# Kernel optimization log

Hardware: AMD Instinct MI355X
Metric: run time of the kernel (lower is better)

The kernel has to match this reference:

```python
import jax, jax.numpy as jnp
import numpy as np

IN_DIMS = [16, 16, 16]
OUT_DIMS = [16, 16, 16]
RANKS = [1, 16, 16, 1]
BATCH = 1024


def setup_inputs() -> dict:
    key = jax.random.key(0)
    ks = jax.random.split(key, 1 + len(IN_DIMS))
    vector = jax.random.normal(ks[0], (BATCH, *IN_DIMS), dtype=jnp.float32)
    inp = {"vector": vector}
    for i in range(len(IN_DIMS)):
        shape = (RANKS[i], OUT_DIMS[i], IN_DIMS[i], RANKS[i + 1])
        scale = 1.0 / float(np.sqrt(RANKS[i] * IN_DIMS[i]))
        inp[f"core{i}"] = jax.random.normal(ks[1 + i], shape, dtype=jnp.float32) * scale
    return inp


def _tt_matvec(vector, cores):
    """y = M @ x where M is the TT/MPO matrix defined by `cores`.

    vector: (B, d_in_1, ..., d_in_d). Returns (B, d_out_1, ..., d_out_d).
    Mirrors TTMatrix.metric_projection exactly (output dims absorbed into batch).
    """
    bs0 = vector.shape[0]
    res = vector[:, None]  # (B, r0=1, d_in_1, ..., d_in_d)
    bs = bs0
    for core in cores:
        r, o, i, k = core.shape
        rem = res.shape[3:]  # remaining un-contracted input dims
        res_t = res.reshape(bs, r, i, -1)  # (bs, r, i, x)
        # contract rank-in and input dim: (r,o,i,k),(b,r,i,x) -> (b,k,o,x)
        new = jnp.einsum('roik,brix->bkox', core, res_t)
        new = jnp.transpose(new, (0, 2, 1, 3)).reshape(bs * o, k, *rem)
        bs = bs * o
        res = new
    res = jnp.squeeze(res, axis=-1)  # last rank is 1
    out_dims = [c.shape[1] for c in cores]
    return res.reshape(bs0, *out_dims)


def reference(vector, core0, core1, core2):
    return _tt_matvec(vector, (core0, core1, core2))
```

## Files before the change

kernel.cpp:

```cpp
#include <hip/hip_runtime.h>
#include <hip/hip_bf16.h>


typedef short bf16x8 __attribute__((ext_vector_type(8)));
typedef float f32x4 __attribute__((ext_vector_type(4)));

#define WS_A1_OFF 0
#define WS_A0_OFF 131072
#define WS_A2_OFF 147456
#define WS_NEEDED 155648

__device__ __forceinline__ unsigned short f2bf(float f) {
    union { float f; unsigned int u; } x; x.f = f;
    unsigned int u = x.u;
    u += 0x7fffu + ((u >> 16) & 1u);
    return (unsigned short)(u >> 16);
}

__device__ __forceinline__ unsigned int pk_bf16(float lo, float hi) {
    __hip_bfloat162 h = __float22bfloat162_rn(make_float2(lo, hi));
    unsigned int r;
    __builtin_memcpy(&r, &h, 4);
    return r;
}

__global__ void tt_repack(const float* __restrict__ c0,
                          const float* __restrict__ c1,
                          const float* __restrict__ c2,
                          unsigned short* __restrict__ ws) {
    int idx = blockIdx.x * 256 + threadIdx.x;
    if (idx < 8192) {
        int o2 = idx >> 9, ks = (idx >> 6) & 7, l = idx & 63;
        int k2 = l & 15;
        unsigned short* dst = ws + ((size_t)(o2 * 8 + ks) * 64 + l) * 8;
        #pragma unroll
        for (int j = 0; j < 8; ++j) {
            int k = ks * 32 + ((l >> 4) * 8) + j;
            dst[j] = f2bf(c1[(k & 15) * 4096 + o2 * 256 + (k >> 4) * 16 + k2]);
        }
    } else if (idx < 9216) {
        int t = idx - 8192;
        int o1 = t >> 6, l = t & 63;
        unsigned short* dst = ws + WS_A0_OFF / 2 + ((size_t)o1 * 64 + l) * 8;
        #pragma unroll
        for (int j = 0; j < 8; ++j) {
            int k = ((l >> 4) * 8) + j;
            float v = (l < 32) ? c0[o1 * 256 + k * 16 + (l & 15)] : 0.f;
            dst[j] = f2bf(v);
        }
    } else if (idx < 9728) {
        int t = idx - 9216;
        int ks = t >> 6, l = t & 63;
        unsigned short* dst = ws + WS_A2_OFF / 2 + ((size_t)ks * 64 + l) * 8;
        #pragma unroll
        for (int j = 0; j < 8; ++j) {
            int k = ks * 32 + ((l >> 4) * 8) + j;
            dst[j] = f2bf(c2[(k & 15) * 256 + (l & 15) * 16 + (k >> 4)]);
        }
    }
}

template <bool PACKED>
__global__ __launch_bounds__(512, 4) void tt_main(
    const float* __restrict__ vg, const float* __restrict__ c0,
    const float* __restrict__ c1, const float* __restrict__ c2,
    const unsigned short* __restrict__ ws, float* __restrict__ outg)
{
    __shared__ unsigned short T1[16384];
    __shared__ unsigned short T2[16384];

    const int b   = blockIdx.x;
    const int t   = threadIdx.x;
    const int w   = t >> 6;
    const int l   = t & 63;
    const int l15 = l & 15;
    const int lg  = l >> 4;

    bf16x8 fb0[2];
    {
        const float* vb = vg + (size_t)b * 4096;
        #pragma unroll
        for (int nt = 0; nt < 2; ++nt) {
            bf16x8 f = {0, 0, 0, 0, 0, 0, 0, 0};
            if (l < 32) {
                int i2 = 2 * w + nt;
                const float* p = vb + (lg * 8) * 256 + i2 * 16 + l15;
                #pragma unroll
                for (int j = 0; j < 8; ++j) f[j] = (short)f2bf(p[j * 256]);
            }
            fb0[nt] = f;
        }
    }
    bf16x8 fa2[8];
    if constexpr (PACKED) {
        #pragma unroll
        for (int ks = 0; ks < 8; ++ks)
            fa2[ks] = *(const bf16x8*)(ws + WS_A2_OFF / 2 + ((size_t)ks * 64 + l) * 8);
    } else {
        for (int ks = 0; ks < 8; ++ks) {
            bf16x8 f;
            for (int j = 0; j < 8; ++j) {
                int k = ks * 32 + lg * 8 + j;
                f[j] = (short)f2bf(c2[(k & 15) * 256 + l15 * 16 + (k >> 4)]);
            }
            fa2[ks] = f;
        }
    }

    const unsigned short* a1p = PACKED ? (ws + (size_t)l * 8) : nullptr;

    for (int nc = 0; nc < 4; ++nc) {
        #pragma unroll
        for (int mtl = 0; mtl < 4; ++mtl) {
            const int o1 = nc * 4 + mtl;
            bf16x8 fa0;
            if constexpr (PACKED) {
                fa0 = *(const bf16x8*)(ws + WS_A0_OFF / 2 + ((size_t)o1 * 64 + l) * 8);
            } else {
                bf16x8 f = {0, 0, 0, 0, 0, 0, 0, 0};
                if (l < 32) {
                    #pragma unroll
                    for (int j = 0; j < 8; ++j)
                        f[j] = (short)f2bf(c0[o1 * 256 + (lg * 8 + j) * 16 + l15]);
                }
                fa0 = f;
            }
            #pragma unroll
            for (int nt = 0; nt < 2; ++nt) {
                f32x4 z = {0.f, 0.f, 0.f, 0.f};
                f32x4 d = __builtin_amdgcn_mfma_f32_16x16x32_bf16(fa0, fb0[nt], z, 0, 0, 0);
                const int i2 = 2 * w + nt;
                const int n  = mtl * 16 + l15;
                int byte = (n * 512 + (i2 * 16 + lg * 4) * 2) ^ ((l15 & 7) << 4);
                uint2 wv;
                wv.x = pk_bf16(d[0], d[1]);
                wv.y = pk_bf16(d[2], d[3]);
                *(uint2*)((char*)T1 + byte) = wv;
            }
        }
        __syncthreads();

        {
            f32x4 acc[2][4];
            #pragma unroll
            for (int rt = 0; rt < 2; ++rt)
                #pragma unroll
                for (int nt = 0; nt < 4; ++nt) acc[rt][nt] = (f32x4){0.f, 0.f, 0.f, 0.f};

            #pragma unroll 2
            for (int ks = 0; ks < 8; ++ks) {
                bf16x8 fa_0, fa_1;
                if constexpr (PACKED) {
                    fa_0 = *(const bf16x8*)(a1p + ((2 * w + 0) * 8 + ks) * 512);
                    fa_1 = *(const bf16x8*)(a1p + ((2 * w + 1) * 8 + ks) * 512);
                } else {
                    bf16x8 ftmp[2];
                    for (int rt = 0; rt < 2; ++rt) {
                        int o2 = 2 * w + rt;
                        bf16x8 f;
                        for (int j = 0; j < 8; ++j) {
                            int k = ks * 32 + lg * 8 + j;
                            f[j] = (short)f2bf(c1[(k & 15) * 4096 + o2 * 256 + (k >> 4) * 16 + l15]);
                        }
                        ftmp[rt] = f;
                    }
                    fa_0 = ftmp[0]; fa_1 = ftmp[1];
                }
                #pragma unroll
                for (int nt = 0; nt < 4; ++nt) {
                    int byte = ((nt * 16 + l15) * 512 + (ks * 32 + lg * 8) * 2) ^ ((l15 & 7) << 4);
                    bf16x8 fb = *(const bf16x8*)((char*)T1 + byte);
                    acc[0][nt] = __builtin_amdgcn_mfma_f32_16x16x32_bf16(fa_0, fb, acc[0][nt], 0, 0, 0);
                    acc[1][nt] = __builtin_amdgcn_mfma_f32_16x16x32_bf16(fa_1, fb, acc[1][nt], 0, 0, 0);
                }
            }
            #pragma unroll
            for (int rt = 0; rt < 2; ++rt) {
                const int o2 = 2 * w + rt;
                #pragma unroll
                for (int nt = 0; nt < 4; ++nt) {
                    int byte = ((nt * 16 + o2) * 512 + (l15 * 16 + lg * 4) * 2) ^ ((o2 & 7) << 4);
                    uint2 wv;
                    wv.x = pk_bf16(acc[rt][nt][0], acc[rt][nt][1]);
                    wv.y = pk_bf16(acc[rt][nt][2], acc[rt][nt][3]);
                    *(uint2*)((char*)T2 + byte) = wv;
                }
            }
        }
        __syncthreads();

        if (w < 4) {
            f32x4 acc3 = {0.f, 0.f, 0.f, 0.f};
            #pragma unroll
            for (int ks = 0; ks < 8; ++ks) {
                int byte = ((w * 16 + l15) * 512 + (ks * 32 + lg * 8) * 2) ^ ((l15 & 7) << 4);
                bf16x8 fb = *(const bf16x8*)((char*)T2 + byte);
                acc3 = __builtin_amdgcn_mfma_f32_16x16x32_bf16(fa2[ks], fb, acc3, 0, 0, 0);
            }
            float* ob = outg + (size_t)b * 4096;
            *(f32x4*)(ob + (nc * 4 + w) * 256 + l15 * 16 + lg * 4) = acc3;
        }
        __syncthreads();
    }
}

extern "C" void kernel_launch(void* const* d_in, const int* in_sizes, int n_in,
                              void* d_out, int out_size, void* d_ws, size_t ws_size,
                              hipStream_t stream) {
    const float* vg  = (const float*)d_in[0];
    const float* c0g = (const float*)d_in[1];
    const float* c1g = (const float*)d_in[2];
    const float* c2g = (const float*)d_in[3];
    float* outg = (float*)d_out;

    const int B = in_sizes[0] / 4096;
    const bool packed = (ws_size >= (size_t)WS_NEEDED) && (d_ws != nullptr);

    if (packed) {
        tt_repack<<<dim3(38), dim3(256), 0, stream>>>(c0g, c1g, c2g, (unsigned short*)d_ws);
        tt_main<true><<<dim3(B), dim3(512), 0, stream>>>(
            vg, c0g, c1g, c2g, (const unsigned short*)d_ws, outg);
    } else {
        tt_main<false><<<dim3(B), dim3(512), 0, stream>>>(
            vg, c0g, c1g, c2g, nullptr, outg);
    }
}
```

Measured before the change: 53.98 us.

## Double-buffer T2, preload core1/core0 fragments, drop trailing barrier

Makes T2 double-buffered so the third stage of one chunk can overlap with the first stage of the next, which lets the trailing __syncthreads be removed. All core1 and core0 fragments for a chunk are now loaded into registers up front, before the MFMA loops, and the stage-2 loop is fully unrolled. Stage 3 splits its accumulation into two independent chains to shorten the MFMA dependency chain. In exchange, register use rises (occupancy hint lowered from 4 to 2 blocks) and LDS use rises by 32KB, which reduces resident blocks per CU.

```diff
diff --git a/kernel.cpp b/kernel.cpp
--- a/kernel.cpp
+++ b/kernel.cpp
@@ -61,13 +61,13 @@
 }
 
 template <bool PACKED>
-__global__ __launch_bounds__(512, 4) void tt_main(
+__global__ __launch_bounds__(512, 2) void tt_main(
     const float* __restrict__ vg, const float* __restrict__ c0,
     const float* __restrict__ c1, const float* __restrict__ c2,
     const unsigned short* __restrict__ ws, float* __restrict__ outg)
 {
     __shared__ unsigned short T1[16384];
-    __shared__ unsigned short T2[16384];
+    __shared__ unsigned short T2[2][16384];
 
     const int b   = blockIdx.x;
     const int t   = threadIdx.x;
@@ -110,25 +110,47 @@
     const unsigned short* a1p = PACKED ? (ws + (size_t)l * 8) : nullptr;
 
     for (int nc = 0; nc < 4; ++nc) {
-        #pragma unroll
-        for (int mtl = 0; mtl < 4; ++mtl) {
-            const int o1 = nc * 4 + mtl;
-            bf16x8 fa0;
-            if constexpr (PACKED) {
-                fa0 = *(const bf16x8*)(ws + WS_A0_OFF / 2 + ((size_t)o1 * 64 + l) * 8);
-            } else {
+        unsigned short* T2c = T2[nc & 1];
+
+        bf16x8 fa1p[16];
+        bf16x8 fa0p[4];
+        if constexpr (PACKED) {
+            #pragma unroll
+            for (int ks = 0; ks < 8; ++ks) {
+                fa1p[ks]     = *(const bf16x8*)(a1p + ((2 * w + 0) * 8 + ks) * 512);
+                fa1p[8 + ks] = *(const bf16x8*)(a1p + ((2 * w + 1) * 8 + ks) * 512);
+            }
+            #pragma unroll
+            for (int mtl = 0; mtl < 4; ++mtl)
+                fa0p[mtl] = *(const bf16x8*)(ws + WS_A0_OFF / 2 +
+                                             ((size_t)(nc * 4 + mtl) * 64 + l) * 8);
+        } else {
+            for (int rt = 0; rt < 2; ++rt)
+                for (int ks = 0; ks < 8; ++ks) {
+                    int o2 = 2 * w + rt;
+                    bf16x8 f;
+                    for (int j = 0; j < 8; ++j) {
+                        int k = ks * 32 + lg * 8 + j;
+                        f[j] = (short)f2bf(c1[(k & 15) * 4096 + o2 * 256 + (k >> 4) * 16 + l15]);
+                    }
+                    fa1p[rt * 8 + ks] = f;
+                }
+            for (int mtl = 0; mtl < 4; ++mtl) {
                 bf16x8 f = {0, 0, 0, 0, 0, 0, 0, 0};
                 if (l < 32) {
-                    #pragma unroll
                     for (int j = 0; j < 8; ++j)
-                        f[j] = (short)f2bf(c0[o1 * 256 + (lg * 8 + j) * 16 + l15]);
-                }
-                fa0 = f;
-            }
+                        f[j] = (short)f2bf(c0[(nc * 4 + mtl) * 256 + (lg * 8 + j) * 16 + l15]);
+                }
+                fa0p[mtl] = f;
+            }
+        }
+
+        #pragma unroll
+        for (int mtl = 0; mtl < 4; ++mtl) {
             #pragma unroll
             for (int nt = 0; nt < 2; ++nt) {
                 f32x4 z = {0.f, 0.f, 0.f, 0.f};
-                f32x4 d = __builtin_amdgcn_mfma_f32_16x16x32_bf16(fa0, fb0[nt], z, 0, 0, 0);
+                f32x4 d = __builtin_amdgcn_mfma_f32_16x16x32_bf16(fa0p[mtl], fb0[nt], z, 0, 0, 0);
                 const int i2 = 2 * w + nt;
                 const int n  = mtl * 16 + l15;
                 int byte = (n * 512 + (i2 * 16 + lg * 4) * 2) ^ ((l15 & 7) << 4);
@@ -147,31 +169,14 @@
                 #pragma unroll
                 for (int nt = 0; nt < 4; ++nt) acc[rt][nt] = (f32x4){0.f, 0.f, 0.f, 0.f};
 
-            #pragma unroll 2
+            #pragma unroll
             for (int ks = 0; ks < 8; ++ks) {
-                bf16x8 fa_0, fa_1;
-                if constexpr (PACKED) {
-                    fa_0 = *(const bf16x8*)(a1p + ((2 * w + 0) * 8 + ks) * 512);
-                    fa_1 = *(const bf16x8*)(a1p + ((2 * w + 1) * 8 + ks) * 512);
-                } else {
-                    bf16x8 ftmp[2];
-                    for (int rt = 0; rt < 2; ++rt) {
-                        int o2 = 2 * w + rt;
-                        bf16x8 f;
-                        for (int j = 0; j < 8; ++j) {
-                            int k = ks * 32 + lg * 8 + j;
-                            f[j] = (short)f2bf(c1[(k & 15) * 4096 + o2 * 256 + (k >> 4) * 16 + l15]);
-                        }
-                        ftmp[rt] = f;
-                    }
-                    fa_0 = ftmp[0]; fa_1 = ftmp[1];
-                }
                 #pragma unroll
                 for (int nt = 0; nt < 4; ++nt) {
                     int byte = ((nt * 16 + l15) * 512 + (ks * 32 + lg * 8) * 2) ^ ((l15 & 7) << 4);
                     bf16x8 fb = *(const bf16x8*)((char*)T1 + byte);
-                    acc[0][nt] = __builtin_amdgcn_mfma_f32_16x16x32_bf16(fa_0, fb, acc[0][nt], 0, 0, 0);
-                    acc[1][nt] = __builtin_amdgcn_mfma_f32_16x16x32_bf16(fa_1, fb, acc[1][nt], 0, 0, 0);
+                    acc[0][nt] = __builtin_amdgcn_mfma_f32_16x16x32_bf16(fa1p[ks],     fb, acc[0][nt], 0, 0, 0);
+                    acc[1][nt] = __builtin_amdgcn_mfma_f32_16x16x32_bf16(fa1p[8 + ks], fb, acc[1][nt], 0, 0, 0);
                 }
             }
             #pragma unroll
@@ -183,24 +188,28 @@
                     uint2 wv;
                     wv.x = pk_bf16(acc[rt][nt][0], acc[rt][nt][1]);
                     wv.y = pk_bf16(acc[rt][nt][2], acc[rt][nt][3]);
-                    *(uint2*)((char*)T2 + byte) = wv;
+                    *(uint2*)((char*)T2c + byte) = wv;
                 }
             }
         }
         __syncthreads();
 
         if (w < 4) {
-            f32x4 acc3 = {0.f, 0.f, 0.f, 0.f};
-            #pragma unroll
-            for (int ks = 0; ks < 8; ++ks) {
-                int byte = ((w * 16 + l15) * 512 + (ks * 32 + lg * 8) * 2) ^ ((l15 & 7) << 4);
-                bf16x8 fb = *(const bf16x8*)((char*)T2 + byte);
-                acc3 = __builtin_amdgcn_mfma_f32_16x16x32_bf16(fa2[ks], fb, acc3, 0, 0, 0);
-            }
+            f32x4 a3a = {0.f, 0.f, 0.f, 0.f};
+            f32x4 a3b = {0.f, 0.f, 0.f, 0.f};
+            #pragma unroll
+            for (int ks = 0; ks < 8; ks += 2) {
+                int byte0 = ((w * 16 + l15) * 512 + ((ks + 0) * 32 + lg * 8) * 2) ^ ((l15 & 7) << 4);
+                int byte1 = ((w * 16 + l15) * 512 + ((ks + 1) * 32 + lg * 8) * 2) ^ ((l15 & 7) << 4);
+                bf16x8 fbA = *(const bf16x8*)((char*)T2c + byte0);
+                bf16x8 fbB = *(const bf16x8*)((char*)T2c + byte1);
+                a3a = __builtin_amdgcn_mfma_f32_16x16x32_bf16(fa2[ks],     fbA, a3a, 0, 0, 0);
+                a3b = __builtin_amdgcn_mfma_f32_16x16x32_bf16(fa2[ks + 1], fbB, a3b, 0, 0, 0);
+            }
+            f32x4 acc3 = a3a + a3b;
             float* ob = outg + (size_t)b * 4096;
             *(f32x4*)(ob + (nc * 4 + w) * 256 + l15 * 16 + lg * 4) = acc3;
         }
-        __syncthreads();
     }
 }
 
```

Result: no change. 55.05 us (+2.0%).
